# Kernel tuning notes

Hardware: AMD Instinct MI355X
Metric: run time of the kernel (lower is better)

The kernel has to match this reference:

```python
import jax, jax.numpy as jnp
import numpy as np

HIDDEN = 4096
SPARSITY_RATIO = 0.1
BLOCK_SIZE = max(1, int(HIDDEN * SPARSITY_RATIO * 2))  # 819, matches torch block_diagonal


def _block_diag_mask(h: int, block_size: int) -> jnp.ndarray:
    # mask[i, j] = True iff i and j fall in the same diagonal block of size block_size
    # (last block may be partial) -- equivalent to the torch loop via floor division
    idx = jnp.arange(h) // block_size
    return idx[:, None] == idx[None, :]


def setup_inputs() -> dict:
    key = jax.random.key(0)
    kx, kw = jax.random.split(key)
    x = jax.random.normal(kx, (8, 2048, HIDDEN), dtype=jnp.float32)
    mask = _block_diag_mask(HIDDEN, BLOCK_SIZE)
    eye = jnp.eye(HIDDEN, dtype=jnp.float32)
    W = eye + 0.1 * jax.random.normal(kw, (HIDDEN, HIDDEN), dtype=jnp.float32)
    # replicate torch init: masked noise on-pattern, identity off-pattern
    W = W * mask.astype(jnp.float32) + eye * (~mask).astype(jnp.float32)
    return {"x": x, "W": W, "mask": mask}


def reference(x, W, mask):
    sparse_W = W * mask.astype(W.dtype)           # [H, H]
    return jnp.einsum('bsh,oh->bso', x, sparse_W)  # x @ sparse_W.T
```

## Files before the change

kernel.cpp:

```cpp
#include <hip/hip_runtime.h>
#include <hip/hip_bf16.h>

#define H       4096
#define BS      819
#define NB      5
#define KPAD    832
#define NPADW   896
#define M_TOTAL 16384
#define XB_LD   (NB * KPAD)
#define NT      (KPAD / 32)
#define BM      256
#define BN      256

typedef __bf16 bf16x8 __attribute__((ext_vector_type(8)));
typedef float  f32x4  __attribute__((ext_vector_type(4)));
typedef float  f32x4u __attribute__((ext_vector_type(4), aligned(4)));

__device__ __forceinline__ void gld_lds16(const void* gptr, void* ldsptr) {
    __builtin_amdgcn_global_load_lds(
        (const __attribute__((address_space(1))) void*)gptr,
        (__attribute__((address_space(3))) void*)ldsptr,
        16, 0, 0);
}

#define PX_GX     3
#define PX_BLOCKS (PX_GX * M_TOTAL)
#define PW_PER_G  ((NPADW * KPAD) / 4 / 256)
#define PW_BLOCKS (PW_PER_G * NB)
#define LC_BLOCKS (M_TOTAL / 256)

__global__ void prep_kernel(const float* __restrict__ x,
                            const float* __restrict__ W,
                            __hip_bfloat16* __restrict__ xb,
                            __hip_bfloat16* __restrict__ wb,
                            float* __restrict__ out) {
    const int bid = blockIdx.x;
    if (bid < PX_BLOCKS) {
        const int m  = bid / PX_GX;
        const int c8 = (bid % PX_GX) * 256 + threadIdx.x;
        if (c8 >= XB_LD / 8) return;
        const int j8 = c8 * 8;
        const int g  = j8 / KPAD;
        const int jj = j8 - g * KPAD;
        const float* xr = x + (size_t)m * H + g * BS;
        union { __hip_bfloat16 h[8]; uint4 u; } v;
        if (jj + 8 <= BS) {
            f32x4u f0 = *reinterpret_cast<const f32x4u*>(xr + jj);
            f32x4u f1 = *reinterpret_cast<const f32x4u*>(xr + jj + 4);
#pragma unroll
            for (int i = 0; i < 4; ++i) {
                v.h[i]     = __float2bfloat16(f0[i]);
                v.h[4 + i] = __float2bfloat16(f1[i]);
            }
        } else {
#pragma unroll
            for (int i = 0; i < 8; ++i) {
                float f = (jj + i < BS) ? xr[jj + i] : 0.f;
                v.h[i] = __float2bfloat16(f);
            }
        }
        *reinterpret_cast<uint4*>(xb + (size_t)m * XB_LD + j8) = v.u;
    } else if (bid < PX_BLOCKS + PW_BLOCKS) {
        const int b   = bid - PX_BLOCKS;
        const int g   = b / PW_PER_G;
        const int t4  = (b - g * PW_PER_G) * 256 + threadIdx.x;
        const int idx = t4 * 4;
        const int n = idx / KPAD;
        const int k = idx - n * KPAD;
        union { __hip_bfloat16 h[4]; uint2 u; } v;
        if (n < BS && k + 4 <= BS) {
            f32x4u f = *reinterpret_cast<const f32x4u*>(W + (size_t)(g * BS + n) * H + g * BS + k);
#pragma unroll
            for (int i = 0; i < 4; ++i) v.h[i] = __float2bfloat16(f[i]);
        } else {
#pragma unroll
            for (int i = 0; i < 4; ++i) {
                float f = 0.f;
                if (n < BS && k + i < BS) f = W[(size_t)(g * BS + n) * H + g * BS + k + i];
                v.h[i] = __float2bfloat16(f);
            }
        }
        *reinterpret_cast<uint2*>(wb + ((size_t)g * NPADW + n) * KPAD + k) = v.u;
    } else {
        const int m = (bid - PX_BLOCKS - PW_BLOCKS) * 256 + threadIdx.x;
        if (m >= M_TOTAL) return;
        const float w = W[(size_t)4095 * H + 4095];
        out[(size_t)m * H + 4095] = x[(size_t)m * H + 4095] * w;
    }
}

__global__ __launch_bounds__(512, 2)
void gemm_kernel(const __hip_bfloat16* __restrict__ xb,
                 const __hip_bfloat16* __restrict__ wb,
                 float* __restrict__ out) {
    __shared__ __hip_bfloat16 sA[4][BM * 32];
    __shared__ __hip_bfloat16 sB[4][BN * 32];

    const int tid  = threadIdx.x;
    const int lane = tid & 63;
    const int wid  = tid >> 6;
    const int wr   = wid >> 2;
    const int wc   = wid & 3;
    const int l16  = lane & 15;
    const int quad = lane >> 4;

    const int mBase = blockIdx.x * BM;
    const int nBase = blockIdx.y * BN;
    const int g     = blockIdx.z;

    const int r0 = tid >> 2;
    const int kc = (tid & 3) ^ ((tid >> 3) & 3);

    const __hip_bfloat16* aSrc0 = xb + (size_t)(mBase + r0      ) * XB_LD + g * KPAD + kc * 8;
    const __hip_bfloat16* aSrc1 = xb + (size_t)(mBase + r0 + 128) * XB_LD + g * KPAD + kc * 8;
    int nrow0 = nBase + r0;        if (nrow0 > NPADW - 1) nrow0 = NPADW - 1;
    int nrow1 = nBase + r0 + 128;  if (nrow1 > NPADW - 1) nrow1 = NPADW - 1;
    const __hip_bfloat16* bSrc0 = wb + ((size_t)g * NPADW + nrow0) * KPAD + kc * 8;
    const __hip_bfloat16* bSrc1 = wb + ((size_t)g * NPADW + nrow1) * KPAD + kc * 8;

    const int dst0 = tid * 16;
    const int dst1 = dst0 + 8192;

    const int cpr  = quad ^ ((l16 >> 1) & 3);
    const int aOff = (wr * 128 + l16) * 32 + cpr * 8;
    const int bOff = (wc * 64  + l16) * 32 + cpr * 8;

    f32x4 acc[8][4] = {};

#define STAGE(t, buf) do {                                       \
        const int koff = (t) * 32;                               \
        gld_lds16(aSrc0 + koff, (char*)sA[(buf)] + dst0);        \
        gld_lds16(aSrc1 + koff, (char*)sA[(buf)] + dst1);        \
        gld_lds16(bSrc0 + koff, (char*)sB[(buf)] + dst0);        \
        gld_lds16(bSrc1 + koff, (char*)sB[(buf)] + dst1);        \
    } while (0)

    STAGE(0, 0);
    STAGE(1, 1);

    for (int t = 0; t < NT; ++t) {
        if (t + 2 < NT) STAGE(t + 2, (t + 2) & 3);
        __builtin_amdgcn_sched_barrier(0);
        if (t + 2 < NT) {
            asm volatile("s_waitcnt vmcnt(8)" ::: "memory");
        } else if (t + 1 < NT) {
            asm volatile("s_waitcnt vmcnt(4)" ::: "memory");
        } else {
            asm volatile("s_waitcnt vmcnt(0)" ::: "memory");
        }
        __builtin_amdgcn_s_barrier();
        __builtin_amdgcn_sched_barrier(0);

        const __hip_bfloat16* A = sA[t & 3];
        const __hip_bfloat16* B = sB[t & 3];
        bf16x8 a[8], b[4];
#pragma unroll
        for (int ni = 0; ni < 4; ++ni)
            b[ni] = *reinterpret_cast<const bf16x8*>(B + bOff + ni * 512);
#pragma unroll
        for (int mi = 0; mi < 8; ++mi)
            a[mi] = *reinterpret_cast<const bf16x8*>(A + aOff + mi * 512);

        __builtin_amdgcn_s_setprio(1);
#pragma unroll
        for (int mi = 0; mi < 8; ++mi)
#pragma unroll
            for (int ni = 0; ni < 4; ++ni)
                acc[mi][ni] = __builtin_amdgcn_mfma_f32_16x16x32_bf16(a[mi], b[ni], acc[mi][ni], 0, 0, 0);
        __builtin_amdgcn_s_setprio(0);
    }
#undef STAGE

    const int orow0 = mBase + wr * 128 + quad * 4;
    const int ocol0 = nBase + wc * 64 + l16;
#pragma unroll
    for (int mi = 0; mi < 8; ++mi) {
#pragma unroll
        for (int ni = 0; ni < 4; ++ni) {
            const int nc = ocol0 + ni * 16;
            if (nc < BS) {
                float* op = out + (size_t)(orow0 + mi * 16) * H + (size_t)g * BS + nc;
#pragma unroll
                for (int r = 0; r < 4; ++r)
                    op[(size_t)r * H] = acc[mi][ni][r];
            }
        }
    }
}

__global__ void fallback_kernel(const float* __restrict__ x,
                                const float* __restrict__ W,
                                float* __restrict__ out) {
    const size_t idx = (size_t)blockIdx.x * blockDim.x + threadIdx.x;
    if (idx >= (size_t)M_TOTAL * H) return;
    const int m = (int)(idx / H);
    const int o = (int)(idx % H);
    const int g = o / BS;
    const int h0 = g * BS;
    const int len = (g < NB) ? BS : 1;
    const float* xr = x + (size_t)m * H + h0;
    const float* wr = W + (size_t)o * H + h0;
    float s = 0.f;
    for (int k = 0; k < len; ++k) s += xr[k] * wr[k];
    out[idx] = s;
}

extern "C" void kernel_launch(void* const* d_in, const int* in_sizes, int n_in,
                              void* d_out, int out_size, void* d_ws, size_t ws_size,
                              hipStream_t stream) {
    const float* x = (const float*)d_in[0];
    const float* W = (const float*)d_in[1];
    float* out = (float*)d_out;

    const size_t xb_elems = (size_t)M_TOTAL * XB_LD;
    const size_t wb_elems = (size_t)NB * NPADW * KPAD;
    const size_t need = (xb_elems + wb_elems) * sizeof(__hip_bfloat16);

    if (ws_size < need) {
        const size_t total = (size_t)M_TOTAL * H;
        fallback_kernel<<<(unsigned)((total + 255) / 256), 256, 0, stream>>>(x, W, out);
        return;
    }

    __hip_bfloat16* xb = (__hip_bfloat16*)d_ws;
    __hip_bfloat16* wb = xb + xb_elems;

    prep_kernel<<<PX_BLOCKS + PW_BLOCKS + LC_BLOCKS, 256, 0, stream>>>(x, W, xb, wb, out);
    gemm_kernel<<<dim3(M_TOTAL / BM, 4, NB), 512, 0, stream>>>(xb, wb, out);
}
```

Before: 662.4 us.

## Restructure GEMM main loop into fine-grained phased pipeline with interleaved loads

```diff
diff --git a/kernel.cpp b/kernel.cpp
--- a/kernel.cpp
+++ b/kernel.cpp
@@ -8,7 +8,6 @@
 #define NPADW   896
 #define M_TOTAL 16384
 #define XB_LD   (NB * KPAD)
-#define NT      (KPAD / 32)
 #define BM      256
 #define BN      256
 
@@ -93,8 +92,8 @@
 void gemm_kernel(const __hip_bfloat16* __restrict__ xb,
                  const __hip_bfloat16* __restrict__ wb,
                  float* __restrict__ out) {
-    __shared__ __hip_bfloat16 sA[4][BM * 32];
-    __shared__ __hip_bfloat16 sB[4][BN * 32];
+    __shared__ __hip_bfloat16 sA[2][2][256 * 32];
+    __shared__ __hip_bfloat16 sB[2][2][256 * 32];
 
     const int tid  = threadIdx.x;
     const int lane = tid & 63;
@@ -108,68 +107,104 @@
     const int nBase = blockIdx.y * BN;
     const int g     = blockIdx.z;
 
-    const int r0 = tid >> 2;
-    const int kc = (tid & 3) ^ ((tid >> 3) & 3);
-
-    const __hip_bfloat16* aSrc0 = xb + (size_t)(mBase + r0      ) * XB_LD + g * KPAD + kc * 8;
-    const __hip_bfloat16* aSrc1 = xb + (size_t)(mBase + r0 + 128) * XB_LD + g * KPAD + kc * 8;
-    int nrow0 = nBase + r0;        if (nrow0 > NPADW - 1) nrow0 = NPADW - 1;
-    int nrow1 = nBase + r0 + 128;  if (nrow1 > NPADW - 1) nrow1 = NPADW - 1;
-    const __hip_bfloat16* bSrc0 = wb + ((size_t)g * NPADW + nrow0) * KPAD + kc * 8;
-    const __hip_bfloat16* bSrc1 = wb + ((size_t)g * NPADW + nrow1) * KPAD + kc * 8;
-
+    const int srow = tid >> 2;
+    const int cg   = (tid & 3) ^ ((tid >> 3) & 3);
+    const __hip_bfloat16* aS0 = xb + (size_t)(mBase + srow) * XB_LD + g * KPAD + cg * 8;
+    const __hip_bfloat16* aS1 = aS0 + (size_t)128 * XB_LD;
+    int nr0 = nBase + srow;        if (nr0 > NPADW - 1) nr0 = NPADW - 1;
+    int nr1 = nBase + srow + 128;  if (nr1 > NPADW - 1) nr1 = NPADW - 1;
+    const __hip_bfloat16* bS0 = wb + ((size_t)g * NPADW + nr0) * KPAD + cg * 8;
+    const __hip_bfloat16* bS1 = wb + ((size_t)g * NPADW + nr1) * KPAD + cg * 8;
     const int dst0 = tid * 16;
     const int dst1 = dst0 + 8192;
 
-    const int cpr  = quad ^ ((l16 >> 1) & 3);
-    const int aOff = (wr * 128 + l16) * 32 + cpr * 8;
-    const int bOff = (wc * 64  + l16) * 32 + cpr * 8;
+#define STAGE_A(BUF, u, kh) do {                                         \
+        gld_lds16(aS0 + (u) * 64 + (kh) * 32, (char*)sA[BUF][kh] + dst0);\
+        gld_lds16(aS1 + (u) * 64 + (kh) * 32, (char*)sA[BUF][kh] + dst1);\
+    } while (0)
+#define STAGE_B(BUF, u, kh) do {                                         \
+        gld_lds16(bS0 + (u) * 64 + (kh) * 32, (char*)sB[BUF][kh] + dst0);\
+        gld_lds16(bS1 + (u) * 64 + (kh) * 32, (char*)sB[BUF][kh] + dst1);\
+    } while (0)
+
+    const int cl16 = (quad ^ ((l16 >> 1) & 3)) * 16;
+    const int aRd  = (wr * 128 + l16) * 64 + cl16;
+    const int bRd  = (wc * 64  + l16) * 64 + cl16;
 
     f32x4 acc[8][4] = {};
-
-#define STAGE(t, buf) do {                                       \
-        const int koff = (t) * 32;                               \
-        gld_lds16(aSrc0 + koff, (char*)sA[(buf)] + dst0);        \
-        gld_lds16(aSrc1 + koff, (char*)sA[(buf)] + dst1);        \
-        gld_lds16(bSrc0 + koff, (char*)sB[(buf)] + dst0);        \
-        gld_lds16(bSrc1 + koff, (char*)sB[(buf)] + dst1);        \
-    } while (0)
-
-    STAGE(0, 0);
-    STAGE(1, 1);
-
-    for (int t = 0; t < NT; ++t) {
-        if (t + 2 < NT) STAGE(t + 2, (t + 2) & 3);
-        __builtin_amdgcn_sched_barrier(0);
-        if (t + 2 < NT) {
-            asm volatile("s_waitcnt vmcnt(8)" ::: "memory");
-        } else if (t + 1 < NT) {
-            asm volatile("s_waitcnt vmcnt(4)" ::: "memory");
-        } else {
-            asm volatile("s_waitcnt vmcnt(0)" ::: "memory");
-        }
-        __builtin_amdgcn_s_barrier();
-        __builtin_amdgcn_sched_barrier(0);
-
-        const __hip_bfloat16* A = sA[t & 3];
-        const __hip_bfloat16* B = sB[t & 3];
-        bf16x8 a[8], b[4];
-#pragma unroll
-        for (int ni = 0; ni < 4; ++ni)
-            b[ni] = *reinterpret_cast<const bf16x8*>(B + bOff + ni * 512);
-#pragma unroll
-        for (int mi = 0; mi < 8; ++mi)
-            a[mi] = *reinterpret_cast<const bf16x8*>(A + aOff + mi * 512);
-
-        __builtin_amdgcn_s_setprio(1);
-#pragma unroll
-        for (int mi = 0; mi < 8; ++mi)
-#pragma unroll
-            for (int ni = 0; ni < 4; ++ni)
-                acc[mi][ni] = __builtin_amdgcn_mfma_f32_16x16x32_bf16(a[mi], b[ni], acc[mi][ni], 0, 0, 0);
-        __builtin_amdgcn_s_setprio(0);
-    }
-#undef STAGE
+    bf16x8 b0, b1, b2, b3;
+
+#define MFMA1(MI, A_) do {                                                           \
+        acc[MI][0] = __builtin_amdgcn_mfma_f32_16x16x32_bf16(A_, b0, acc[MI][0],0,0,0);\
+        acc[MI][1] = __builtin_amdgcn_mfma_f32_16x16x32_bf16(A_, b1, acc[MI][1],0,0,0);\
+        acc[MI][2] = __builtin_amdgcn_mfma_f32_16x16x32_bf16(A_, b2, acc[MI][2],0,0,0);\
+        acc[MI][3] = __builtin_amdgcn_mfma_f32_16x16x32_bf16(A_, b3, acc[MI][3],0,0,0);\
+    } while (0)
+
+    #define PH(BUF, KK, HH, STG, VM) do {                                            \
+        bf16x8 a0_, a1_, a2_, a3_;                                                   \
+        {   const char* p_ = (const char*)sA[BUF][KK] + aRd + (HH) * 4096;           \
+            a0_ = *(const bf16x8*)(p_);                                              \
+            a1_ = *(const bf16x8*)(p_ + 1024);                                       \
+            a2_ = *(const bf16x8*)(p_ + 2048);                                       \
+            a3_ = *(const bf16x8*)(p_ + 3072); }                                     \
+        if ((HH) == 0) {                                                             \
+            const char* q_ = (const char*)sB[BUF][KK] + bRd;                         \
+            b0 = *(const bf16x8*)(q_);                                               \
+            b1 = *(const bf16x8*)(q_ + 1024);                                        \
+            b2 = *(const bf16x8*)(q_ + 2048);                                        \
+            b3 = *(const bf16x8*)(q_ + 3072); }                                      \
+        STG;                                                                         \
+        __builtin_amdgcn_s_barrier();                                                \
+        __builtin_amdgcn_s_setprio(1);                                               \
+        MFMA1((HH) * 4 + 0, a0_);                                                    \
+        MFMA1((HH) * 4 + 1, a1_);                                                    \
+        MFMA1((HH) * 4 + 2, a2_);                                                    \
+        MFMA1((HH) * 4 + 3, a3_);                                                    \
+        __builtin_amdgcn_s_setprio(0);                                               \
+        asm volatile("s_waitcnt vmcnt(" VM ")" ::: "memory");                        \
+        __builtin_amdgcn_s_barrier();                                                \
+    } while (0)
+
+    STAGE_A(0, 0, 0);
+    STAGE_B(0, 0, 0);
+    STAGE_A(0, 0, 1);
+    STAGE_B(0, 0, 1);
+    STAGE_A(1, 1, 0);
+    STAGE_B(1, 1, 0);
+    asm volatile("s_waitcnt vmcnt(8)" ::: "memory");
+    __builtin_amdgcn_s_barrier();
+
+    for (int i = 0; i < 5; ++i) {
+        const int t1 = 2 * i + 1, t2 = 2 * i + 2, t3 = 2 * i + 3;
+        PH(0, 0, 0, STAGE_A(1, t1, 1), "8");
+        PH(0, 0, 1, STAGE_B(1, t1, 1), "8");
+        PH(0, 1, 0, STAGE_A(0, t2, 0), "8");
+        PH(0, 1, 1, STAGE_B(0, t2, 0), "8");
+        PH(1, 0, 0, STAGE_A(0, t2, 1), "8");
+        PH(1, 0, 1, STAGE_B(0, t2, 1), "8");
+        PH(1, 1, 0, STAGE_A(1, t3, 0), "8");
+        PH(1, 1, 1, STAGE_B(1, t3, 0), "8");
+    }
+
+    PH(0, 0, 0, STAGE_A(1, 11, 1), "8");
+    PH(0, 0, 1, STAGE_B(1, 11, 1), "8");
+    PH(0, 1, 0, STAGE_A(0, 12, 0), "8");
+    PH(0, 1, 1, STAGE_B(0, 12, 0), "8");
+    PH(1, 0, 0, STAGE_A(0, 12, 1), "8");
+    PH(1, 0, 1, STAGE_B(0, 12, 1), "8");
+    PH(1, 1, 0, { }, "8");
+    PH(1, 1, 1, { }, "4");
+
+    PH(0, 0, 0, { }, "4");
+    PH(0, 0, 1, { }, "0");
+    PH(0, 1, 0, { }, "0");
+    PH(0, 1, 1, { }, "0");
+
+#undef PH
+#undef MFMA1
+#undef STAGE_A
+#undef STAGE_B
 
     const int orow0 = mBase + wr * 128 + quad * 4;
     const int ocol0 = nBase + wc * 64 + l16;
```

Result: no change. 661.9 us (-0.1%).
